# Kernel optimization log

Measured on AMD Instinct MI355X. Metric: run time of the kernel, lower is better.

Reference implementation:

```python
import jax, jax.numpy as jnp
import numpy as np

H = 16      # query heads
KVH = 4     # kv heads
G = H // KVH


def _split_heads(x, nh, d):
    # [b, P, C, nh*d] -> [b, nh, P, C, d]
    b, P, C, _ = x.shape
    return jnp.transpose(x.reshape(b, P, C, nh, d), (0, 3, 1, 2, 4))


def _rel_shift(x, P, T):
    # x: [b, h, T, P]  (Transformer-XL style relative shift via memory reinterpretation)
    b, h = x.shape[:2]
    xv = x.reshape(b, h, P, T)
    xp = jnp.concatenate([jnp.zeros((b, h, P, 1), x.dtype), xv], axis=-1)  # [b,h,P,T+1]
    return xp.reshape(b, h, T + 1, P)[:, :, 1:, :]


def _rel_shift_chan(x, C, T):
    # x: [b, h, T, C]; gather with index (C-1 - |i-j|) tiled over T rows
    i = jnp.arange(C)
    idx = (C - 1) - jnp.abs(i[:, None] - i[None, :])          # [C, C]
    tiled = jnp.tile(idx, (T // C, 1))[None, None]            # [1,1,T,C]
    return jnp.take_along_axis(x, jnp.broadcast_to(tiled, x.shape), axis=-1)


def _forward(hidden_states, positional_embedding, channel_embedding,
             Wq, Wkv, Wpos, Wchan, Wproj, attn_bias):
    b, P, C, E = hidden_states.shape
    D = E // H
    EKV = D * KVH
    T = P * C

    q = hidden_states @ Wq                                    # [b,P,C,E]
    kv = hidden_states @ Wkv                                  # [b,P,C,2*EKV]
    gk_raw, v_raw = kv[..., :EKV], kv[..., EKV:]
    tk_raw = positional_embedding @ Wpos                      # [1,P,1,EKV]
    ck_raw = channel_embedding @ Wchan                        # [1,1,C,EKV]

    q = _split_heads(q, H, D)                                 # [b,H,P,C,D]
    gk = jnp.repeat(_split_heads(gk_raw, KVH, D), G, axis=1)  # [b,H,P,C,D]
    v = jnp.repeat(_split_heads(v_raw, KVH, D), G, axis=1)    # [b,H,P,C,D]
    tk = jnp.repeat(_split_heads(tk_raw, KVH, D), G, axis=1)[:, :, :, 0, :]  # [1,H,P,D]
    ck = jnp.repeat(_split_heads(ck_raw, KVH, D), G, axis=1)[:, :, 0, :, :]  # [1,H,C,D]

    gb, tb, cb = (jnp.repeat(attn_bias[i * EKV:(i + 1) * EKV].reshape(KVH, D), G, axis=0)
                  [None, :, None, None, :] for i in range(3))  # each [1,H,1,1,D]

    qg = (q + gb).reshape(b, H, T, D)
    qt = (q + tb).reshape(b, H, T, D)
    qc = (q + cb).reshape(b, H, T, D)

    gk_f = gk.reshape(b, H, T, D)
    global_att = jnp.einsum('bhtd,bhsd->bhts', qg, gk_f)      # [b,H,T,T]
    time_att = jnp.einsum('bhtd,bhpd->bhtp', qt, tk)          # [b,H,T,P]
    chan_att = jnp.einsum('bhtd,bhcd->bhtc', qc, ck)          # [b,H,T,C]

    time_att = _rel_shift(time_att, P, T)
    chan_att = _rel_shift_chan(chan_att, C, T)

    # repeat_channel + repeat_time -> both [b,H,T,T]
    attn = jnp.repeat(time_att, C, axis=-1) + jnp.tile(chan_att, (1, 1, 1, P))

    # global window mask (+/-10 in time, all-true for last chan_len rows)
    pm = jnp.tril(jnp.ones((P, P), bool), 10) & jnp.triu(jnp.ones((P, P), bool), -10)
    wm = jnp.repeat(jnp.repeat(pm, C, axis=0), C, axis=1)
    wm = wm.at[-C:].set(True)
    attn = attn + jnp.where(wm, global_att, jnp.zeros((), attn.dtype))

    attn = attn / jnp.asarray(D ** 0.5, attn.dtype)           # scale_attn_weights

    causal = jnp.repeat(jnp.repeat(jnp.tril(jnp.ones((P, P), bool)), C, axis=0), C, axis=1)
    attn = jnp.where(causal, attn, jnp.finfo(attn.dtype).min)

    w = jax.nn.softmax(attn, axis=-1)                         # [b,H,T,T]
    out = jnp.einsum('bhts,bhsd->bhtd', w, v.reshape(b, H, T, D)).reshape(b, H, P, C, D)

    # merge heads: [b,H,P,C,D] -> [b,P,C,E], then output proj
    out = jnp.transpose(out, (0, 2, 3, 1, 4)).reshape(b, P, C, E)
    return out @ Wproj


def setup_inputs() -> dict:
    key = jax.random.key(0)
    ks = jax.random.split(key, 9)
    B, P, C, E, EKV = 2, 128, 8, 1024, 256
    s = 0.02
    return {
        'hidden_states': jax.random.normal(ks[0], (B, P, C, E), jnp.float32),
        'positional_embedding': jax.random.normal(ks[1], (1, P, 1, E), jnp.float32),
        'channel_embedding': jax.random.normal(ks[2], (1, 1, C, E), jnp.float32),
        'Wq': jax.random.normal(ks[3], (E, E), jnp.float32) * s,
        'Wkv': jax.random.normal(ks[4], (E, 2 * EKV), jnp.float32) * s,
        'Wpos': jax.random.normal(ks[5], (E, EKV), jnp.float32) * s,
        'Wchan': jax.random.normal(ks[6], (E, EKV), jnp.float32) * s,
        'Wproj': jax.random.normal(ks[7], (E, E), jnp.float32) * s,
        'attn_bias': jax.random.normal(ks[8], (3 * EKV,), jnp.float32) * s,
    }


def reference(hidden_states, positional_embedding, channel_embedding,
              Wq, Wkv, Wpos, Wchan, Wproj, attn_bias):
    return _forward(hidden_states, positional_embedding, channel_embedding,
                    Wq, Wkv, Wpos, Wchan, Wproj, attn_bias)
```

## Files before the change

### kernel.cpp

```cpp
#include <hip/hip_runtime.h>
#include <hip/hip_bf16.h>

#define BB 2
#define PP 128
#define CC 8
#define EE 1024
#define HH 16
#define KVHH 4
#define DD 64
#define TT 1024
#define EKVV 256

typedef unsigned short u16;
typedef unsigned int u32;
typedef __attribute__((ext_vector_type(8))) short bf16x8;
typedef __attribute__((ext_vector_type(4))) float f32x4;

__device__ __forceinline__ float b2f(u16 u) {
    u32 x = ((u32)u) << 16;
    return __uint_as_float(x);
}
__device__ __forceinline__ u16 f2b(float f) {
    u32 x = __float_as_uint(f);
    u32 r = (x + 0x7FFFu + ((x >> 16) & 1u)) >> 16;
    return (u16)r;
}

template <int CTRL>
__device__ __forceinline__ float dpp_mv(float v) {
    return __int_as_float(__builtin_amdgcn_update_dpp(
        __float_as_int(v), __float_as_int(v), CTRL, 0xF, 0xF, true));
}
__device__ __forceinline__ float red_max16(float v) {
    v = fmaxf(v, dpp_mv<0xB1>(v));
    v = fmaxf(v, dpp_mv<0x4E>(v));
    v = fmaxf(v, dpp_mv<0x141>(v));
    v = fmaxf(v, dpp_mv<0x140>(v));
    return v;
}
__device__ __forceinline__ float red_sum16(float v) {
    v += dpp_mv<0xB1>(v);
    v += dpp_mv<0x4E>(v);
    v += dpp_mv<0x141>(v);
    v += dpp_mv<0x140>(v);
    return v;
}

#define GLL16(gp, lp)                                                          \
    __builtin_amdgcn_global_load_lds(                                          \
        (__attribute__((address_space(1))) void*)(gp),                         \
        (__attribute__((address_space(3))) void*)(lp), 16, 0, 0)

__global__ __launch_bounds__(256) void k_prep(const float* __restrict__ hidden,
                                              const float* __restrict__ Wq,
                                              const float* __restrict__ Wkv,
                                              const float* __restrict__ Wproj,
                                              const float* __restrict__ pos,
                                              const float* __restrict__ chan,
                                              const float* __restrict__ Wpos,
                                              const float* __restrict__ Wchan,
                                              u16* __restrict__ hb,
                                              u16* __restrict__ btq,
                                              u16* __restrict__ btp,
                                              float* __restrict__ tkb,
                                              float* __restrict__ ckb) {
    __shared__ __align__(16) char sm[8704];
    int bid = blockIdx.x;
    int tid = threadIdx.x;

    if (bid < 96) {
        int tile = bid >> 3, kh = bid & 7;
        float (*As)[68] = (float (*)[68])sm;
        float (*Bs)[68] = (float (*)[68])(sm + 4352);
        const float* A; const float* B; float* C; int M, m0, n0;
        if (tile < 8) { A = pos;  B = Wpos;  C = tkb + kh * 32768; M = 128; m0 = (tile >> 2) * 64; n0 = (tile & 3) * 64; }
        else          { A = chan; B = Wchan; C = ckb + kh * 2048;  M = 8;   m0 = 0;               n0 = (tile - 8) * 64; }
        int tx = tid & 15, ty = tid >> 4;
        float acc[4][4];
#pragma unroll
        for (int r = 0; r < 4; r++)
#pragma unroll
            for (int c = 0; c < 4; c++) acc[r][c] = 0.f;
        int am = tid >> 2, ak = (tid & 3) << 2;
        int bk = tid >> 4, bn = (tid & 15) << 2;
        for (int k0 = kh * 128; k0 < kh * 128 + 128; k0 += 16) {
            int row = m0 + am;
            float4 av;
            if (row < M) av = *reinterpret_cast<const float4*>(A + (size_t)row * 1024 + k0 + ak);
            else av = make_float4(0.f, 0.f, 0.f, 0.f);
            As[ak + 0][am] = av.x;
            As[ak + 1][am] = av.y;
            As[ak + 2][am] = av.z;
            As[ak + 3][am] = av.w;
            float4 bv = *reinterpret_cast<const float4*>(B + (size_t)(k0 + bk) * 256 + n0 + bn);
            Bs[bk][bn + 0] = bv.x;
            Bs[bk][bn + 1] = bv.y;
            Bs[bk][bn + 2] = bv.z;
            Bs[bk][bn + 3] = bv.w;
            __syncthreads();
#pragma unroll
            for (int kk = 0; kk < 16; kk++) {
                float4 a4 = *reinterpret_cast<const float4*>(&As[kk][ty << 2]);
                float4 b4 = *reinterpret_cast<const float4*>(&Bs[kk][tx << 2]);
                acc[0][0] += a4.x * b4.x; acc[0][1] += a4.x * b4.y; acc[0][2] += a4.x * b4.z; acc[0][3] += a4.x * b4.w;
                acc[1][0] += a4.y * b4.x; acc[1][1] += a4.y * b4.y; acc[1][2] += a4.y * b4.z; acc[1][3] += a4.y * b4.w;
                acc[2][0] += a4.z * b4.x; acc[2][1] += a4.z * b4.y; acc[2][2] += a4.z * b4.z; acc[2][3] += a4.z * b4.w;
                acc[3][0] += a4.w * b4.x; acc[3][1] += a4.w * b4.y; acc[3][2] += a4.w * b4.z; acc[3][3] += a4.w * b4.w;
            }
            __syncthreads();
        }
#pragma unroll
        for (int r = 0; r < 4; r++) {
            int row = m0 + (ty << 2) + r;
            if (row < M) {
#pragma unroll
                for (int c = 0; c < 4; c++) {
                    int col = n0 + (tx << 2) + c;
                    C[(size_t)row * 256 + col] = acc[r][c];
                }
            }
        }
        return;
    }
    bid -= 96;
    if (bid < 1024) {
        int base = (bid * 256 + tid) * 8;
        float4 a0 = *(const float4*)(hidden + base);
        float4 a1 = *(const float4*)(hidden + base + 4);
        u16 o[8] = {f2b(a0.x), f2b(a0.y), f2b(a0.z), f2b(a0.w),
                    f2b(a1.x), f2b(a1.y), f2b(a1.z), f2b(a1.w)};
        *(uint4*)(hb + base) = *(uint4*)o;
        return;
    }
    bid -= 1024;
    const float* W;
    u16* out;
    int N, tk, tn;
    if (bid < 1024) {
        W = Wq; out = btq; N = 1024; tk = bid >> 5; tn = bid & 31;
    } else if (bid < 1536) {
        int b2 = bid - 1024;
        W = Wkv; out = btq + 1024 * 1024; N = 512; tk = b2 >> 4; tn = b2 & 15;
    } else {
        int b2 = bid - 1536;
        W = Wproj; out = btp; N = 1024; tk = b2 >> 5; tn = b2 & 31;
    }
    float (*ts)[33] = (float (*)[33])sm;
    int r = tid >> 3, c4 = (tid & 7) << 2;
    float4 v = *(const float4*)(W + (size_t)(tk * 32 + r) * N + tn * 32 + c4);
    ts[r][c4 + 0] = v.x;
    ts[r][c4 + 1] = v.y;
    ts[r][c4 + 2] = v.z;
    ts[r][c4 + 3] = v.w;
    __syncthreads();
    u16 o[4] = {f2b(ts[c4 + 0][r]), f2b(ts[c4 + 1][r]),
                f2b(ts[c4 + 2][r]), f2b(ts[c4 + 3][r])};
    *(ushort4*)(out + (size_t)(tn * 32 + r) * 1024 + tk * 32 + c4) = *(ushort4*)o;
}

__global__ __launch_bounds__(256) void mgemm_qkv2(const u16* __restrict__ Ab,
                                                  const u16* __restrict__ BT,
                                                  u16* __restrict__ qout,
                                                  u16* __restrict__ kvout,
                                                  u16* __restrict__ vtb,
                                                  const float* __restrict__ tkb,
                                                  const float* __restrict__ ckb,
                                                  u16* __restrict__ tkr,
                                                  float* __restrict__ ckr) {
    __shared__ __align__(16) u16 As[2][128 * 32];
    __shared__ __align__(16) u16 Bs[2][128 * 32];
    int tid = threadIdx.x;
    int ntile = blockIdx.x;

    if (ntile == 12) {
        int y = blockIdx.y;
        int p = y * 8 + (tid >> 5), col = (tid & 31) << 3;
        float s0 = 0.f, s1 = 0.f, s2 = 0.f, s3 = 0.f,
              s4 = 0.f, s5 = 0.f, s6 = 0.f, s7 = 0.f;
#pragma unroll
        for (int sl = 0; sl < 8; sl++) {
            const float* tp = tkb + sl * 32768 + p * 256 + col;
            float4 a0 = *(const float4*)(tp);
            float4 a1 = *(const float4*)(tp + 4);
            s0 += a0.x; s1 += a0.y; s2 += a0.z; s3 += a0.w;
            s4 += a1.x; s5 += a1.y; s6 += a1.z; s7 += a1.w;
        }
        u16 o[8] = {f2b(s0), f2b(s1), f2b(s2), f2b(s3),
                    f2b(s4), f2b(s5), f2b(s6), f2b(s7)};
        int kvh = col >> 6, d = col & 63;
        *(uint4*)(tkr + kvh * 8192 + p * 64 + d) = *(uint4*)o;
        if (y == 0) {
            int c = tid >> 5, cc = (tid & 31) << 3;
            float t[8];
#pragma unroll
            for (int j = 0; j < 8; j++) t[j] = 0.f;
#pragma unroll
            for (int sl = 0; sl < 8; sl++) {
                const float* cp = ckb + sl * 2048 + c * 256 + cc;
                float4 a0 = *(const float4*)(cp);
                float4 a1 = *(const float4*)(cp + 4);
                t[0] += a0.x; t[1] += a0.y; t[2] += a0.z; t[3] += a0.w;
                t[4] += a1.x; t[5] += a1.y; t[6] += a1.z; t[7] += a1.w;
            }
            int kvh2 = cc >> 6, d2 = cc & 63;
            float* op = ckr + kvh2 * 512 + c * 64 + d2;
            *(float4*)(op)     = make_float4(t[0], t[1], t[2], t[3]);
            *(float4*)(op + 4) = make_float4(t[4], t[5], t[6], t[7]);
        }
        return;
    }

    int m0 = blockIdx.y * 128;
    int n0g = ntile * 128;
    u16* Cout; int BN, n0;
    if (ntile < 8) { Cout = qout;  BN = 1024; n0 = n0g; }
    else           { Cout = kvout; BN = 512;  n0 = n0g - 1024; }

    int lane = tid & 63, wave = tid >> 6;
    int r16 = lane & 15, quad = lane >> 4;
    int mb = (wave >> 1) * 64, nb = (wave & 1) * 64;
    int srow = tid >> 2, skg = (tid & 3) << 3;

#define STAGE_QKV(buf, k0)                                                         \
    do {                                                                           \
        GLL16(Ab + (size_t)(m0 + srow) * 1024 + (k0) + skg,      As[buf] + tid * 8);        \
        GLL16(Ab + (size_t)(m0 + srow + 64) * 1024 + (k0) + skg, As[buf] + (tid + 256) * 8);\
        GLL16(BT + (size_t)(n0g + srow) * 1024 + (k0) + skg,      Bs[buf] + tid * 8);       \
        GLL16(BT + (size_t)(n0g + srow + 64) * 1024 + (k0) + skg, Bs[buf] + (tid + 256) * 8);\
    } while (0)

    f32x4 acc[4][4];
#pragma unroll
    for (int mt = 0; mt < 4; mt++)
#pragma unroll
        for (int nt = 0; nt < 4; nt++) acc[mt][nt] = (f32x4){0.f, 0.f, 0.f, 0.f};

    STAGE_QKV(0, 0);
    __syncthreads();
    int cur = 0;
    for (int k0 = 0; k0 < 1024; k0 += 32) {
        if (k0 + 32 < 1024) STAGE_QKV(cur ^ 1, k0 + 32);
        bf16x8 af[4], bfr[4];
#pragma unroll
        for (int mt = 0; mt < 4; mt++)
            af[mt] = *(const bf16x8*)(As[cur] + (mb + mt * 16 + r16) * 32 + quad * 8);
#pragma unroll
        for (int nt = 0; nt < 4; nt++)
            bfr[nt] = *(const bf16x8*)(Bs[cur] + (nb + nt * 16 + r16) * 32 + quad * 8);
#pragma unroll
        for (int mt = 0; mt < 4; mt++)
#pragma unroll
            for (int nt = 0; nt < 4; nt++)
                acc[mt][nt] = __builtin_amdgcn_mfma_f32_16x16x32_bf16(af[mt], bfr[nt], acc[mt][nt], 0, 0, 0);
        __syncthreads();
        cur ^= 1;
    }
    if (ntile < 10) {
#pragma unroll
        for (int mt = 0; mt < 4; mt++)
#pragma unroll
            for (int nt = 0; nt < 4; nt++)
#pragma unroll
                for (int rg = 0; rg < 4; rg++) {
                    int row = m0 + mb + mt * 16 + quad * 4 + rg;
                    int col = n0 + nb + nt * 16 + r16;
                    Cout[(size_t)row * BN + col] = f2b(acc[mt][nt][rg]);
                }
    } else {
#pragma unroll
        for (int mt = 0; mt < 4; mt++)
#pragma unroll
            for (int nt = 0; nt < 4; nt++)
#pragma unroll
                for (int rg = 0; rg < 4; rg++) {
                    int row = m0 + mb + mt * 16 + quad * 4 + rg;
                    int col = n0 + nb + nt * 16 + r16;
                    int bb = row >> 10, s = row & 1023;
                    vtb[((size_t)bb << 18) + ((size_t)(col - 256) << 10) + s] =
                        f2b(acc[mt][nt][rg]);
                }
    }
#undef STAGE_QKV
}

__global__ __launch_bounds__(256) void mgemm_proj2(const u16* __restrict__ Ab,
                                                   const u16* __restrict__ BT,
                                                   float* __restrict__ Cf) {
    __shared__ __align__(16) u16 As[2][128 * 32];
    __shared__ __align__(16) u16 Bs[2][64 * 32];
    int tid = threadIdx.x;
    int n0 = blockIdx.x * 64;
    int m0 = blockIdx.y * 128;

    int lane = tid & 63, wave = tid >> 6;
    int r16 = lane & 15, quad = lane >> 4;
    int mb = (wave >> 1) * 64, nb = (wave & 1) * 32;
    int srow = tid >> 2, skg = (tid & 3) << 3;

#define STAGE_PRJ(buf, k0)                                                         \
    do {                                                                           \
        GLL16(Ab + (size_t)(m0 + srow) * 1024 + (k0) + skg,      As[buf] + tid * 8);        \
        GLL16(Ab + (size_t)(m0 + srow + 64) * 1024 + (k0) + skg, As[buf] + (tid + 256) * 8);\
        GLL16(BT + (size_t)(n0 + srow) * 1024 + (k0) + skg,      Bs[buf] + tid * 8);        \
    } while (0)

    f32x4 acc[4][2];
#pragma unroll
    for (int mt = 0; mt < 4; mt++)
#pragma unroll
        for (int nt = 0; nt < 2; nt++) acc[mt][nt] = (f32x4){0.f, 0.f, 0.f, 0.f};

    STAGE_PRJ(0, 0);
    __syncthreads();
    int cur = 0;
    for (int k0 = 0; k0 < 1024; k0 += 32) {
        if (k0 + 32 < 1024) STAGE_PRJ(cur ^ 1, k0 + 32);
        bf16x8 af[4], bfr[2];
#pragma unroll
        for (int mt = 0; mt < 4; mt++)
            af[mt] = *(const bf16x8*)(As[cur] + (mb + mt * 16 + r16) * 32 + quad * 8);
#pragma unroll
        for (int nt = 0; nt < 2; nt++)
            bfr[nt] = *(const bf16x8*)(Bs[cur] + (nb + nt * 16 + r16) * 32 + quad * 8);
#pragma unroll
        for (int mt = 0; mt < 4; mt++)
#pragma unroll
            for (int nt = 0; nt < 2; nt++)
                acc[mt][nt] = __builtin_amdgcn_mfma_f32_16x16x32_bf16(af[mt], bfr[nt], acc[mt][nt], 0, 0, 0);
        __syncthreads();
        cur ^= 1;
    }
#pragma unroll
    for (int mt = 0; mt < 4; mt++)
#pragma unroll
        for (int nt = 0; nt < 2; nt++)
#pragma unroll
            for (int rg = 0; rg < 4; rg++) {
                int row = m0 + mb + mt * 16 + quad * 4 + rg;
                int col = n0 + nb + nt * 16 + r16;
                Cf[(size_t)row * 1024 + col] = acc[mt][nt][rg];
            }
#undef STAGE_PRJ
}

__global__ __launch_bounds__(256, 2) void k_att4(const u16* __restrict__ qb,
                                                 const u16* __restrict__ kvb,
                                                 const u16* __restrict__ vt,
                                                 const u16* __restrict__ tkr,
                                                 const float* __restrict__ ckr,
                                                 const float* __restrict__ bias,
                                                 u16* __restrict__ A2) {
    __shared__ __align__(16) char smem[75520];
    u16*   taX  = (u16*)(smem);
    u16*   qg   = (u16*)(smem);
    u16*   Kst  = (u16*)(smem + 17408);
    u16*   Pst  = (u16*)(smem + 35840);
    u16*   Vst  = (u16*)(smem + 53248);
    float* csA  = (float*)(smem + 70912);
    float* cks  = (float*)(smem + 72960);
    float* cbmg = (float*)(smem + 75008);
    float* tbv  = (float*)(smem + 75264);

    int tid = threadIdx.x;
    int lane = tid & 63, wave = tid >> 6;
    int r16 = lane & 15, quad = lane >> 4;
    int gx = blockIdx.x, h = blockIdx.y, b = blockIdx.z;
    int g = ((h ^ b) & 1) ? (15 - gx) : gx;
    int kvh = h >> 2;
    int t0 = g * 64;
    int nch = (g + 2) >> 1;

    const u16* vptr = vt + ((size_t)(b * KVHH + kvh)) * DD * TT
                    + (size_t)(tid >> 4) * TT + ((tid & 15) << 3);
    const u16* kptr = kvb + ((size_t)(b * TT) + (tid >> 3)) * (2 * EKVV)
                    + kvh * 64 + ((tid & 7) << 3);

    uint4 V0g, V1g, V2g, V3g, K0g, K1g, K2g, K3g;
    bool pk_next;

#define PRE(c0p)                                                               \
    do {                                                                       \
        V0g = *(const uint4*)(vptr + (c0p));                                   \
        V1g = *(const uint4*)(vptr + 16 * TT + (c0p));                         \
        V2g = *(const uint4*)(vptr + 32 * TT + (c0p));                         \
        V3g = *(const uint4*)(vptr + 48 * TT + (c0p));                         \
        pk_next = (g == 15) || ((c0p) + 128 > g * 64 - 80);                    \
        if (pk_next) {                                                         \
            const u16* kp_ = kptr + (size_t)(c0p) * (2 * EKVV);                \
            K0g = *(const uint4*)(kp_);                                        \
            K1g = *(const uint4*)(kp_ + 32 * 2 * EKVV);                        \
            K2g = *(const uint4*)(kp_ + 64 * 2 * EKVV);                        \
            K3g = *(const uint4*)(kp_ + 96 * 2 * EKVV);                        \
        }                                                                      \
    } while (0)

    PRE(0);

#pragma unroll
    for (int i = 0; i < 2; i++) {
        int idx = tid + i * 256;
        int row = idx >> 3, dg = (idx & 7) << 3;
        uint4 u = *(const uint4*)(qb + ((size_t)(b * TT + t0 + row)) * EE + h * 64 + dg);
        u16 tmp[8]; *(uint4*)tmp = u;
        u16 o[8];
#pragma unroll
        for (int j = 0; j < 8; j++) o[j] = f2b(b2f(tmp[j]) + bias[kvh * 64 + dg + j]);
        *(uint4*)(qg + row * 72 + dg) = *(uint4*)o;
    }
    if (tid < 64) {
        cbmg[tid] = bias[2 * EKVV + kvh * 64 + tid] - bias[kvh * 64 + tid];
        tbv[tid]  = bias[EKVV + kvh * 64 + tid];
    }
#pragma unroll
    for (int i = 0; i < 2; i++) {
        int idx = tid + i * 256;
        cks[idx] = ckr[kvh * 512 + idx];
    }
    __syncthreads();

    {
        int row = tid >> 2, cA = (tid & 3) << 1;
        int rm8 = row & 7;
        int d0 = rm8 - cA;       if (d0 < 0) d0 = -d0;
        int d1 = rm8 - (cA + 1); if (d1 < 0) d1 = -d1;
        const float* k0p = cks + (7 - d0) * 64;
        const float* k1p = cks + (7 - d1) * 64;
        float a0 = 0.f, a1 = 0.f;
#pragma unroll 8
        for (int d = 0; d < 64; d++) {
            float qv = b2f(qg[row * 72 + d]) + cbmg[d];
            a0 += qv * k0p[d];
            a1 += qv * k1p[d];
        }
        csA[row * 8 + cA] = a0;
        csA[row * 8 + cA + 1] = a1;
    }

    bf16x8 aq0 = *(const bf16x8*)(qg + (wave * 16 + r16) * 72 + quad * 8);
    bf16x8 aq1 = *(const bf16x8*)(qg + (wave * 16 + r16) * 72 + 32 + quad * 8);
    bf16x8 aqt0, aqt1;
    {
        const u16* qrow = qb + ((size_t)(b * TT + t0 + wave * 16 + r16)) * EE + h * 64;
        uint4 u0 = *(const uint4*)(qrow + quad * 8);
        uint4 u1 = *(const uint4*)(qrow + 32 + quad * 8);
        u16 t0v[8], t1v[8]; *(uint4*)t0v = u0; *(uint4*)t1v = u1;
        u16 o0[8], o1[8];
#pragma unroll
        for (int j = 0; j < 8; j++) {
            o0[j] = f2b(b2f(t0v[j]) + tbv[quad * 8 + j]);
            o1[j] = f2b(b2f(t1v[j]) + tbv[32 + quad * 8 + j]);
        }
        aqt0 = *(bf16x8*)o0;
        aqt1 = *(bf16x8*)o1;
    }

    {
        const u16* tkp = tkr + kvh * 8192;
#pragma unroll
        for (int i = 0; i < 4; i++) {
            int idx = tid + i * 256;
            int p = idx >> 3, dg = (idx & 7) << 3;
            *(uint4*)(Kst + p * 72 + dg) = *(const uint4*)(tkp + p * 64 + dg);
        }
    }
    __syncthreads();

    int rpi_w = (t0 >> 3) + wave * 2 + (quad >> 1);
    int xsh = rpi_w - 127;
#pragma unroll
    for (int nt = 0; nt < 8; nt++) {
        const u16* kp = Kst + (nt * 16 + r16) * 72 + quad * 8;
        bf16x8 b0 = *(const bf16x8*)(kp);
        bf16x8 b1 = *(const bf16x8*)(kp + 32);
        f32x4 a = {0.f, 0.f, 0.f, 0.f};
        a = __builtin_amdgcn_mfma_f32_16x16x32_bf16(aqt0, b0, a, 0, 0, 0);
        a = __builtin_amdgcn_mfma_f32_16x16x32_bf16(aqt1, b1, a, 0, 0, 0);
        int x = nt * 16 + r16 + xsh;
        if (x >= 0) {
            u16 o4[4] = {f2b(a[0]), f2b(a[1]), f2b(a[2]), f2b(a[3])};
            *(ushort4*)(taX + x * 68 + wave * 16 + quad * 4) = *(ushort4*)o4;
        }
    }

    float m[4], l[4];
    f32x4 accv[4];
#pragma unroll
    for (int rg = 0; rg < 4; rg++) { m[rg] = -1.0e30f; l[rg] = 0.f; }
#pragma unroll
    for (int nt = 0; nt < 4; nt++) accv[nt] = (f32x4){0.f, 0.f, 0.f, 0.f};

    int rowbase = wave * 16 + quad * 4;
    int rpi[4];
#pragma unroll
    for (int rg = 0; rg < 4; rg++) rpi[rg] = (t0 + rowbase + rg) >> 3;

    for (int ci = 0; ci < nch; ci++) {
        int c0 = ci * 128;
        bool pk = pk_next;
        __syncthreads();
        {
            u16* vw = Vst + (tid >> 4) * 138 + ((tid & 15) << 3);
            *(uint4*)(vw)            = V0g;
            *(uint4*)(vw + 16 * 138) = V1g;
            *(uint4*)(vw + 32 * 138) = V2g;
            *(uint4*)(vw + 48 * 138) = V3g;
            if (pk) {
                u16* kw = Kst + (tid >> 3) * 72 + ((tid & 7) << 3);
                *(uint4*)(kw)           = K0g;
                *(uint4*)(kw + 32 * 72) = K1g;
                *(uint4*)(kw + 64 * 72) = K2g;
                *(uint4*)(kw + 96 * 72) = K3g;
            }
        }
        if (ci + 1 < nch) PRE((ci + 1) * 128);
        __syncthreads();

        bool pkq = (c0 + 128 > g * 64 - 80) || (g == 15 && wave == 3);
        f32x4 sc[8];
        if (pkq) {
            __builtin_amdgcn_s_setprio(1);
#pragma unroll
            for (int nt = 0; nt < 8; nt++) {
                const u16* kp = Kst + (nt * 16 + r16) * 72 + quad * 8;
                bf16x8 b0 = *(const bf16x8*)(kp);
                bf16x8 b1 = *(const bf16x8*)(kp + 32);
                f32x4 a = {0.f, 0.f, 0.f, 0.f};
                a = __builtin_amdgcn_mfma_f32_16x16x32_bf16(aq0, b0, a, 0, 0, 0);
                a = __builtin_amdgcn_mfma_f32_16x16x32_bf16(aq1, b1, a, 0, 0, 0);
                sc[nt] = a;
            }
            __builtin_amdgcn_s_setprio(0);
        } else {
#pragma unroll
            for (int nt = 0; nt < 8; nt++) sc[nt] = (f32x4){0.f, 0.f, 0.f, 0.f};
        }

        float csr[4];
#pragma unroll
        for (int rg = 0; rg < 4; rg++) csr[rg] = csA[(rowbase + rg) * 8 + (r16 & 7)];
        int c08 = c0 >> 3;
#pragma unroll
        for (int nt = 0; nt < 8; nt++) {
            int spi = c08 + 2 * nt + (r16 >> 3);
            ushort4 t4 = *(const ushort4*)(taX + spi * 68 + rowbase);
            float tsv[4] = {b2f(t4.x), b2f(t4.y), b2f(t4.z), b2f(t4.w)};
#pragma unroll
            for (int rg = 0; rg < 4; rg++) {
                bool win = (rpi[rg] == 127) || (rpi[rg] - spi <= 10);
                float scv = ((win ? sc[nt][rg] : 0.f) + tsv[rg] + csr[rg]) * 0.125f;
                sc[nt][rg] = (spi <= rpi[rg]) ? scv : -1.0e30f;
            }
        }

        float cm[4], alpha[4], psum[4];
#pragma unroll
        for (int rg = 0; rg < 4; rg++) {
            float v = sc[0][rg];
#pragma unroll
            for (int nt = 1; nt < 8; nt++) v = fmaxf(v, sc[nt][rg]);
            v = red_max16(v);
            float mn = fmaxf(m[rg], v);
            alpha[rg] = __expf(m[rg] - mn);
            m[rg] = mn;
            cm[rg] = mn;
        }
#pragma unroll
        for (int rg = 0; rg < 4; rg++) psum[rg] = 0.f;
#pragma unroll
        for (int nt = 0; nt < 8; nt++)
#pragma unroll
            for (int rg = 0; rg < 4; rg++) {
                float e = __expf(sc[nt][rg] - cm[rg]);
                sc[nt][rg] = e;
                psum[rg] += e;
            }
#pragma unroll
        for (int rg = 0; rg < 4; rg++) {
            psum[rg] = red_sum16(psum[rg]);
            l[rg] = l[rg] * alpha[rg] + psum[rg];
        }
#pragma unroll
        for (int nt = 0; nt < 4; nt++)
#pragma unroll
            for (int rg = 0; rg < 4; rg++) accv[nt][rg] *= alpha[rg];

#pragma unroll
        for (int nt = 0; nt < 8; nt++)
#pragma unroll
            for (int rg = 0; rg < 4; rg++)
                Pst[(rowbase + rg) * 136 + nt * 16 + r16] = f2b(sc[nt][rg]);

        __builtin_amdgcn_s_setprio(1);
#pragma unroll
        for (int ks = 0; ks < 4; ks++) {
            bf16x8 ap = *(const bf16x8*)(Pst + (wave * 16 + r16) * 136 + ks * 32 + quad * 8);
#pragma unroll
            for (int nt = 0; nt < 4; nt++) {
                bf16x8 bv = *(const bf16x8*)(Vst + (nt * 16 + r16) * 138 + ks * 32 + quad * 8);
                accv[nt] = __builtin_amdgcn_mfma_f32_16x16x32_bf16(ap, bv, accv[nt], 0, 0, 0);
            }
        }
        __builtin_amdgcn_s_setprio(0);
    }
#undef PRE

#pragma unroll
    for (int nt = 0; nt < 4; nt++)
#pragma unroll
        for (int rg = 0; rg < 4; rg++) {
            int rt = t0 + rowbase + rg;
            A2[((size_t)(b * TT + rt)) * EE + h * 64 + nt * 16 + r16] =
                f2b(accv[nt][rg] / l[rg]);
        }
}

extern "C" void kernel_launch(void* const* d_in, const int* in_sizes, int n_in,
                              void* d_out, int out_size, void* d_ws, size_t ws_size,
                              hipStream_t stream) {
    const float* hidden = (const float*)d_in[0];
    const float* pos    = (const float*)d_in[1];
    const float* chan   = (const float*)d_in[2];
    const float* Wq     = (const float*)d_in[3];
    const float* Wkv    = (const float*)d_in[4];
    const float* Wpos   = (const float*)d_in[5];
    const float* Wchan  = (const float*)d_in[6];
    const float* Wproj  = (const float*)d_in[7];
    const float* bias   = (const float*)d_in[8];

    u16* qb    = (u16*)d_ws;
    u16* kvb   = qb + 2097152;
    u16* A2    = kvb + 1048576;
    u16* vt    = A2 + 2097152;
    u16* hb    = vt + 524288;
    u16* btq   = hb + 2097152;
    u16* btp   = btq + 1572864;
    u16* tkr   = btp + 1048576;
    float* tkb = (float*)(tkr + 32768);
    float* ckb = tkb + 262144;
    float* ckr = ckb + 16384;

    dim3 blk(256);
    k_prep<<<3680, blk, 0, stream>>>(hidden, Wq, Wkv, Wproj, pos, chan, Wpos, Wchan,
                                     hb, btq, btp, tkb, ckb);
    mgemm_qkv2<<<dim3(13, 16), blk, 0, stream>>>(hb, btq, qb, kvb, vt,
                                                 tkb, ckb, tkr, ckr);
    k_att4<<<dim3(16, 16, 2), blk, 0, stream>>>(qb, kvb, vt, tkr, ckr, bias, A2);
    mgemm_proj2<<<dim3(16, 16), blk, 0, stream>>>(A2, btp, (float*)d_out);
}
```

Before: 175.0 us.

## Split long causal attention rows across two blocks with flash-decoding merge kernel

The attention kernel now uses 64-key chunks instead of 128. Query tiles 8-15, which have the most causal work, are split into two blocks over halves of the key range. A lookup table balances work across 24 blocks per head. The split blocks write unnormalized accumulators plus running max and sum to workspace, and a new merge kernel combines them into the output. Shared memory use drops so three blocks fit per CU, at the cost of an extra launch, more global traffic for the partials, and more loop iterations.

```diff
diff --git a/kernel.cpp b/kernel.cpp
--- a/kernel.cpp
+++ b/kernel.cpp
@@ -343,58 +343,66 @@
 #undef STAGE_PRJ
 }
 
-__global__ __launch_bounds__(256, 2) void k_att4(const u16* __restrict__ qb,
+__global__ __launch_bounds__(256, 3) void k_att4(const u16* __restrict__ qb,
                                                  const u16* __restrict__ kvb,
                                                  const u16* __restrict__ vt,
                                                  const u16* __restrict__ tkr,
                                                  const float* __restrict__ ckr,
                                                  const float* __restrict__ bias,
-                                                 u16* __restrict__ A2) {
-    __shared__ __align__(16) char smem[75520];
+                                                 u16* __restrict__ A2,
+                                                 float* __restrict__ pacc,
+                                                 float* __restrict__ pml) {
+    __shared__ __align__(16) char smem[49664];
     u16*   taX  = (u16*)(smem);
     u16*   qg   = (u16*)(smem);
+    u16*   tkS  = (u16*)(smem + 17408);
     u16*   Kst  = (u16*)(smem + 17408);
+    u16*   Vst  = (u16*)(smem + 26624);
     u16*   Pst  = (u16*)(smem + 35840);
-    u16*   Vst  = (u16*)(smem + 53248);
-    float* csA  = (float*)(smem + 70912);
-    float* cks  = (float*)(smem + 72960);
-    float* cbmg = (float*)(smem + 75008);
-    float* tbv  = (float*)(smem + 75264);
+    float* csA  = (float*)(smem + 45056);
+    float* cks  = (float*)(smem + 47104);
+    float* cbmg = (float*)(smem + 49152);
+    float* tbv  = (float*)(smem + 49408);
+
+    static const unsigned char Gt[24] = {15,15,14,14,13,13,12,12,
+                                          7, 6,11,11,10,10, 9, 5,
+                                          0, 1, 2, 8, 3, 9, 8, 4};
+    static const unsigned char Mt[24] = {0,1,1,0,0,1,1,0,
+                                         2,2,0,1,1,0,0,2,
+                                         2,2,2,0,2,1,1,2};
 
     int tid = threadIdx.x;
     int lane = tid & 63, wave = tid >> 6;
     int r16 = lane & 15, quad = lane >> 4;
-    int gx = blockIdx.x, h = blockIdx.y, b = blockIdx.z;
-    int g = ((h ^ b) & 1) ? (15 - gx) : gx;
+    int h = blockIdx.y, b = blockIdx.z;
+    int g = Gt[blockIdx.x], mode = Mt[blockIdx.x];
     int kvh = h >> 2;
     int t0 = g * 64;
-    int nch = (g + 2) >> 1;
+    int hn = (g + 1) >> 1;
+    int clo = (mode == 1) ? hn : 0;
+    int chi = (mode == 0) ? hn : (g + 1);
 
     const u16* vptr = vt + ((size_t)(b * KVHH + kvh)) * DD * TT
-                    + (size_t)(tid >> 4) * TT + ((tid & 15) << 3);
+                    + (size_t)(tid >> 3) * TT + ((tid & 7) << 3);
     const u16* kptr = kvb + ((size_t)(b * TT) + (tid >> 3)) * (2 * EKVV)
                     + kvh * 64 + ((tid & 7) << 3);
 
-    uint4 V0g, V1g, V2g, V3g, K0g, K1g, K2g, K3g;
+    uint4 V0g, V1g, K0g, K1g;
     bool pk_next;
 
 #define PRE(c0p)                                                               \
     do {                                                                       \
         V0g = *(const uint4*)(vptr + (c0p));                                   \
-        V1g = *(const uint4*)(vptr + 16 * TT + (c0p));                         \
-        V2g = *(const uint4*)(vptr + 32 * TT + (c0p));                         \
-        V3g = *(const uint4*)(vptr + 48 * TT + (c0p));                         \
-        pk_next = (g == 15) || ((c0p) + 128 > g * 64 - 80);                    \
+        V1g = *(const uint4*)(vptr + 32 * TT + (c0p));                         \
+        pk_next = (g == 15) || ((c0p) + 136 > g * 64);                         \
         if (pk_next) {                                                         \
             const u16* kp_ = kptr + (size_t)(c0p) * (2 * EKVV);                \
             K0g = *(const uint4*)(kp_);                                        \
             K1g = *(const uint4*)(kp_ + 32 * 2 * EKVV);                        \
-            K2g = *(const uint4*)(kp_ + 64 * 2 * EKVV);                        \
-            K3g = *(const uint4*)(kp_ + 96 * 2 * EKVV);                        \
         }                                                                      \
     } while (0)
 
-    PRE(0);
+    PRE(clo * 64);
 
 #pragma unroll
     for (int i = 0; i < 2; i++) {
@@ -460,7 +468,7 @@
         for (int i = 0; i < 4; i++) {
             int idx = tid + i * 256;
             int p = idx >> 3, dg = (idx & 7) << 3;
-            *(uint4*)(Kst + p * 72 + dg) = *(const uint4*)(tkp + p * 64 + dg);
+            *(uint4*)(tkS + p * 72 + dg) = *(const uint4*)(tkp + p * 64 + dg);
         }
     }
     __syncthreads();
@@ -469,7 +477,7 @@
     int xsh = rpi_w - 127;
 #pragma unroll
     for (int nt = 0; nt < 8; nt++) {
-        const u16* kp = Kst + (nt * 16 + r16) * 72 + quad * 8;
+        const u16* kp = tkS + (nt * 16 + r16) * 72 + quad * 8;
         bf16x8 b0 = *(const bf16x8*)(kp);
         bf16x8 b1 = *(const bf16x8*)(kp + 32);
         f32x4 a = {0.f, 0.f, 0.f, 0.f};
@@ -494,33 +502,29 @@
 #pragma unroll
     for (int rg = 0; rg < 4; rg++) rpi[rg] = (t0 + rowbase + rg) >> 3;
 
-    for (int ci = 0; ci < nch; ci++) {
-        int c0 = ci * 128;
+    for (int ci = clo; ci < chi; ci++) {
+        int c0 = ci * 64;
         bool pk = pk_next;
         __syncthreads();
         {
-            u16* vw = Vst + (tid >> 4) * 138 + ((tid & 15) << 3);
-            *(uint4*)(vw)            = V0g;
-            *(uint4*)(vw + 16 * 138) = V1g;
-            *(uint4*)(vw + 32 * 138) = V2g;
-            *(uint4*)(vw + 48 * 138) = V3g;
+            u16* vw = Vst + (tid >> 3) * 72 + ((tid & 7) << 3);
+            *(uint4*)(vw)           = V0g;
+            *(uint4*)(vw + 32 * 72) = V1g;
             if (pk) {
                 u16* kw = Kst + (tid >> 3) * 72 + ((tid & 7) << 3);
                 *(uint4*)(kw)           = K0g;
                 *(uint4*)(kw + 32 * 72) = K1g;
-                *(uint4*)(kw + 64 * 72) = K2g;
-                *(uint4*)(kw + 96 * 72) = K3g;
-            }
-        }
-        if (ci + 1 < nch) PRE((ci + 1) * 128);
+            }
+        }
+        if (ci + 1 < chi) PRE((ci + 1) * 64);
         __syncthreads();
 
-        bool pkq = (c0 + 128 > g * 64 - 80) || (g == 15 && wave == 3);
-        f32x4 sc[8];
+        bool pkq = (c0 + 136 - 16 * wave > g * 64) || (g == 15 && wave == 3);
+        f32x4 sc[4];
         if (pkq) {
             __builtin_amdgcn_s_setprio(1);
 #pragma unroll
-            for (int nt = 0; nt < 8; nt++) {
+            for (int nt = 0; nt < 4; nt++) {
                 const u16* kp = Kst + (nt * 16 + r16) * 72 + quad * 8;
                 bf16x8 b0 = *(const bf16x8*)(kp);
                 bf16x8 b1 = *(const bf16x8*)(kp + 32);
@@ -532,7 +536,7 @@
             __builtin_amdgcn_s_setprio(0);
         } else {
 #pragma unroll
-            for (int nt = 0; nt < 8; nt++) sc[nt] = (f32x4){0.f, 0.f, 0.f, 0.f};
+            for (int nt = 0; nt < 4; nt++) sc[nt] = (f32x4){0.f, 0.f, 0.f, 0.f};
         }
 
         float csr[4];
@@ -540,7 +544,7 @@
         for (int rg = 0; rg < 4; rg++) csr[rg] = csA[(rowbase + rg) * 8 + (r16 & 7)];
         int c08 = c0 >> 3;
 #pragma unroll
-        for (int nt = 0; nt < 8; nt++) {
+        for (int nt = 0; nt < 4; nt++) {
             int spi = c08 + 2 * nt + (r16 >> 3);
             ushort4 t4 = *(const ushort4*)(taX + spi * 68 + rowbase);
             float tsv[4] = {b2f(t4.x), b2f(t4.y), b2f(t4.z), b2f(t4.w)};
@@ -557,7 +561,7 @@
         for (int rg = 0; rg < 4; rg++) {
             float v = sc[0][rg];
 #pragma unroll
-            for (int nt = 1; nt < 8; nt++) v = fmaxf(v, sc[nt][rg]);
+            for (int nt = 1; nt < 4; nt++) v = fmaxf(v, sc[nt][rg]);
             v = red_max16(v);
             float mn = fmaxf(m[rg], v);
             alpha[rg] = __expf(m[rg] - mn);
@@ -567,7 +571,7 @@
 #pragma unroll
         for (int rg = 0; rg < 4; rg++) psum[rg] = 0.f;
 #pragma unroll
-        for (int nt = 0; nt < 8; nt++)
+        for (int nt = 0; nt < 4; nt++)
 #pragma unroll
             for (int rg = 0; rg < 4; rg++) {
                 float e = __expf(sc[nt][rg] - cm[rg]);
@@ -585,18 +589,18 @@
             for (int rg = 0; rg < 4; rg++) accv[nt][rg] *= alpha[rg];
 
 #pragma unroll
-        for (int nt = 0; nt < 8; nt++)
+        for (int nt = 0; nt < 4; nt++)
 #pragma unroll
             for (int rg = 0; rg < 4; rg++)
-                Pst[(rowbase + rg) * 136 + nt * 16 + r16] = f2b(sc[nt][rg]);
+                Pst[(rowbase + rg) * 72 + nt * 16 + r16] = f2b(sc[nt][rg]);
 
         __builtin_amdgcn_s_setprio(1);
 #pragma unroll
-        for (int ks = 0; ks < 4; ks++) {
-            bf16x8 ap = *(const bf16x8*)(Pst + (wave * 16 + r16) * 136 + ks * 32 + quad * 8);
+        for (int ks = 0; ks < 2; ks++) {
+            bf16x8 ap = *(const bf16x8*)(Pst + (wave * 16 + r16) * 72 + ks * 32 + quad * 8);
 #pragma unroll
             for (int nt = 0; nt < 4; nt++) {
-                bf16x8 bv = *(const bf16x8*)(Vst + (nt * 16 + r16) * 138 + ks * 32 + quad * 8);
+                bf16x8 bv = *(const bf16x8*)(Vst + (nt * 16 + r16) * 72 + ks * 32 + quad * 8);
                 accv[nt] = __builtin_amdgcn_mfma_f32_16x16x32_bf16(ap, bv, accv[nt], 0, 0, 0);
             }
         }
@@ -604,14 +608,64 @@
     }
 #undef PRE
 
-#pragma unroll
-    for (int nt = 0; nt < 4; nt++)
-#pragma unroll
-        for (int rg = 0; rg < 4; rg++) {
-            int rt = t0 + rowbase + rg;
-            A2[((size_t)(b * TT + rt)) * EE + h * 64 + nt * 16 + r16] =
-                f2b(accv[nt][rg] / l[rg]);
-        }
+    if (mode == 2) {
+#pragma unroll
+        for (int nt = 0; nt < 4; nt++)
+#pragma unroll
+            for (int rg = 0; rg < 4; rg++) {
+                int rt = t0 + rowbase + rg;
+                A2[((size_t)(b * TT + rt)) * EE + h * 64 + nt * 16 + r16] =
+                    f2b(accv[nt][rg] / l[rg]);
+            }
+    } else {
+        int slot = ((b * 16 + h) * 8 + (g - 8)) * 2 + mode;
+        float* pa = pacc + (size_t)slot * 4096;
+#pragma unroll
+        for (int nt = 0; nt < 4; nt++)
+#pragma unroll
+            for (int rg = 0; rg < 4; rg++)
+                pa[(rowbase + rg) * 64 + nt * 16 + r16] = accv[nt][rg];
+        if (r16 == 0) {
+#pragma unroll
+            for (int rg = 0; rg < 4; rg++) {
+                pml[slot * 128 + rowbase + rg]      = m[rg];
+                pml[slot * 128 + 64 + rowbase + rg] = l[rg];
+            }
+        }
+    }
+}
+
+__global__ __launch_bounds__(256) void k_merge(const float* __restrict__ pacc,
+                                               const float* __restrict__ pml,
+                                               u16* __restrict__ A2) {
+    int tid = threadIdx.x;
+    int x = blockIdx.x, h = blockIdx.y, b = blockIdx.z;
+    int g = 8 + x;
+    int slot = ((b * 16 + h) * 8 + x) * 2;
+    const float* a0 = pacc + (size_t)slot * 4096;
+    const float* a1 = a0 + 4096;
+    const float* ml0 = pml + slot * 128;
+    const float* ml1 = ml0 + 128;
+    int row = tid >> 2, seg = (tid & 3) << 4;
+    float m0 = ml0[row], l0 = ml0[64 + row];
+    float m1 = ml1[row], l1 = ml1[64 + row];
+    float M = fmaxf(m0, m1);
+    float e0 = __expf(m0 - M), e1 = __expf(m1 - M);
+    float inv = 1.f / (l0 * e0 + l1 * e1);
+    u16 o[16];
+#pragma unroll
+    for (int j0 = 0; j0 < 16; j0 += 4) {
+        float4 v0 = *(const float4*)(a0 + row * 64 + seg + j0);
+        float4 v1 = *(const float4*)(a1 + row * 64 + seg + j0);
+        o[j0 + 0] = f2b((v0.x * e0 + v1.x * e1) * inv);
+        o[j0 + 1] = f2b((v0.y * e0 + v1.y * e1) * inv);
+        o[j0 + 2] = f2b((v0.z * e0 + v1.z * e1) * inv);
+        o[j0 + 3] = f2b((v0.w * e0 + v1.w * e1) * inv);
+    }
+    int rt = g * 64 + row;
+    u16* outp = A2 + ((size_t)(b * TT + rt)) * EE + h * 64 + seg;
+    *(uint4*)(outp)     = *(uint4*)o;
+    *(uint4*)(outp + 8) = *(uint4*)(o + 8);
 }
 
 extern "C" void kernel_launch(void* const* d_in, const int* in_sizes, int n_in,
@@ -638,12 +692,16 @@
     float* tkb = (float*)(tkr + 32768);
     float* ckb = tkb + 262144;
     float* ckr = ckb + 16384;
+    float* pacc = ckr + 2048;
+    float* pml  = pacc + 2097152;
 
     dim3 blk(256);
     k_prep<<<3680, blk, 0, stream>>>(hidden, Wq, Wkv, Wproj, pos, chan, Wpos, Wchan,
                                      hb, btq, btp, tkb, ckb);
     mgemm_qkv2<<<dim3(13, 16), blk, 0, stream>>>(hb, btq, qb, kvb, vt,
                                                  tkb, ckb, tkr, ckr);
-    k_att4<<<dim3(16, 16, 2), blk, 0, stream>>>(qb, kvb, vt, tkr, ckr, bias, A2);
+    k_att4<<<dim3(24, 16, 2), blk, 0, stream>>>(qb, kvb, vt, tkr, ckr, bias, A2,
+                                                pacc, pml);
+    k_merge<<<dim3(8, 16, 2), blk, 0, stream>>>(pacc, pml, A2);
     mgemm_proj2<<<dim3(16, 16), blk, 0, stream>>>(A2, btp, (float*)d_out);
 }
```

New measurement: 162.7 us. 7.0% less time.
